# Performance work log

Measured on AMD Instinct MI355X. Metric: run time of the kernel, lower is better.

## Reference

```python
import jax, jax.numpy as jnp
import numpy as np

NUM_CANDIDATES = 9
CENTER_IN_GT = True
MIN_IOU = 0.0
LEVELS = [262144, 32768, 4096, 512]  # anchors per FPN level (static)
NUM_GT = 64


def _to_box(c, s):
    lo = c - s / 2
    hi = c + s / 2
    # layout [x1, y1, x2, y2, z1, z2]
    return jnp.stack([lo[:, 0], lo[:, 1], hi[:, 0], hi[:, 1], lo[:, 2], hi[:, 2]], axis=1)


def setup_inputs() -> dict:
    key = jax.random.key(0)
    k1, k2, k3, k4 = jax.random.split(key, 4)
    n = sum(LEVELS)
    a_ctr = jax.random.uniform(k1, (n, 3), dtype=jnp.float32) * 512.0
    a_sz = jax.random.uniform(k2, (n, 3), dtype=jnp.float32) * 60.0 + 4.0
    g_ctr = jax.random.uniform(k3, (NUM_GT, 3), dtype=jnp.float32) * 512.0
    g_sz = jax.random.uniform(k4, (NUM_GT, 3), dtype=jnp.float32) * 90.0 + 10.0
    return {"gt_boxes": _to_box(g_ctr, g_sz), "anchors": _to_box(a_ctr, a_sz)}


def _centers(b):
    return jnp.stack([(b[:, 0] + b[:, 2]) / 2,
                      (b[:, 1] + b[:, 3]) / 2,
                      (b[:, 4] + b[:, 5]) / 2], axis=1)


def _iou(a, b):
    # a: (N,6), b: (M,6) -> (N,M) 3D IoU
    def vol(x):
        return (x[:, 2] - x[:, 0]) * (x[:, 3] - x[:, 1]) * (x[:, 5] - x[:, 4])
    v1, v2 = vol(a), vol(b)
    wx = jnp.clip(jnp.minimum(a[:, None, 2], b[None, :, 2]) - jnp.maximum(a[:, None, 0], b[None, :, 0]), 0.0)
    wy = jnp.clip(jnp.minimum(a[:, None, 3], b[None, :, 3]) - jnp.maximum(a[:, None, 1], b[None, :, 1]), 0.0)
    wz = jnp.clip(jnp.minimum(a[:, None, 5], b[None, :, 5]) - jnp.maximum(a[:, None, 4], b[None, :, 4]), 0.0)
    inter = wx * wy * wz
    return inter / (v1[:, None] + v2[None, :] - inter + 1e-6)


def reference(gt_boxes, anchors):
    n = anchors.shape[0]
    m = gt_boxes.shape[0]
    a_ctr = _centers(anchors)   # (N,3)
    g_ctr = _centers(gt_boxes)  # (M,3)

    # squared center distance (monotone in L2 distance, so topk ordering identical)
    d2 = ((a_ctr * a_ctr).sum(1)[:, None] + (g_ctr * g_ctr).sum(1)[None, :]
          - 2.0 * a_ctr @ g_ctr.T)  # (N,M)

    # per-level, per-GT top-k nearest anchors -> candidate set (vectorized over all GTs)
    cand_mask = jnp.zeros((n, m), dtype=bool)
    cand_idx_list = []
    gt_ids = jnp.arange(m)[:, None]
    start = 0
    for lvl in LEVELS:
        k = min(NUM_CANDIDATES, lvl)
        d_lvl = d2[start:start + lvl].T            # (M, lvl)
        _, idx = jax.lax.top_k(-d_lvl, k)          # smallest distances
        gidx = idx + start                         # (M, k) global anchor ids
        cand_mask = cand_mask.at[gidx, gt_ids].set(True)
        cand_idx_list.append(gidx)
        start += lvl
    cand_idx = jnp.concatenate(cand_idx_list, axis=1)  # (M, K_total)

    iou = _iou(anchors, gt_boxes)  # (N,M)

    # adaptive threshold per GT: mean + std (torch default: unbiased) over candidates
    cand_iou = jnp.take_along_axis(iou.T, cand_idx, axis=1)  # (M, K_total)
    thr = jnp.maximum(cand_iou.mean(axis=1) + cand_iou.std(axis=1, ddof=1), MIN_IOU)  # (M,)

    pos = cand_mask & (iou >= thr[None, :])
    if CENTER_IN_GT:
        inside = ((a_ctr[:, None, 0] >= gt_boxes[None, :, 0]) & (a_ctr[:, None, 0] <= gt_boxes[None, :, 2]) &
                  (a_ctr[:, None, 1] >= gt_boxes[None, :, 1]) & (a_ctr[:, None, 1] <= gt_boxes[None, :, 3]) &
                  (a_ctr[:, None, 2] >= gt_boxes[None, :, 4]) & (a_ctr[:, None, 2] <= gt_boxes[None, :, 5]))
        pos = pos & inside

    # conflict resolution: the sequential GT loop in the original assigns each anchor
    # to the positive GT with the highest IoU (ties -> earliest GT index) == argmax.
    any_pos = pos.any(axis=1)
    masked_iou = jnp.where(pos, iou, -jnp.inf)
    best = jnp.argmax(masked_iou, axis=1)  # (N,)
    matched_iou = jnp.where(any_pos, jnp.take_along_axis(iou, best[:, None], axis=1)[:, 0], 0.0)
    matched_gt_indices = jnp.where(any_pos, best, -1).astype(jnp.int32)
    labels = (matched_gt_indices >= 0).astype(jnp.int32)
    return matched_gt_indices, matched_iou, labels
```

## Files before the change

### kernel.cpp

```cpp
#include <hip/hip_runtime.h>
#include <cstdint>


#define NCAND 36
#define QCAP 64
#define OVF  0x80000000u
#define LVL1_START 262144
#define LVL2_START 294912
#define LVL3_START 299008
#define SEG0 512
#define SEG1 64

__device__ __constant__ int   c_lvl_start[2] = {0, 262144};
__device__ __constant__ int   c_lvl_end[2]   = {262144, 294912};
__device__ __constant__ float c_T[2] = {961.0f, 3844.0f};

__device__ inline unsigned f2ord(float f) {
    unsigned u = __float_as_uint(f);
    return (u & 0x80000000u) ? ~u : (u | 0x80000000u);
}

__global__ void scanK(const float* __restrict__ anchors, const float* __restrict__ gt_boxes,
                      unsigned long long* __restrict__ l0, unsigned long long* __restrict__ l1,
                      unsigned* __restrict__ c0, unsigned* __restrict__ c1,
                      unsigned long long* __restrict__ packed, int n, int m) {
    int b    = blockIdx.x;
    int tid  = threadIdx.x;
    int base = b << 9;
    int lvl  = (base >= LVL1_START) ? 1 : 0;
    float T  = c_T[lvl];

    int segN = (lvl == 0) ? SEG0 : SEG1;
    int seg  = (lvl == 0) ? b : (b - SEG0);
    unsigned long long* lseg = (lvl == 0) ? l0 : l1;

    __shared__ float4 gt4[64];
    __shared__ unsigned qcnt[64];

    if (tid < 64) {
        qcnt[tid] = 0;
        if (tid < m) {
            int g = tid;
            float gx = (gt_boxes[g*6+0] + gt_boxes[g*6+2]) * 0.5f;
            float gy = (gt_boxes[g*6+1] + gt_boxes[g*6+3]) * 0.5f;
            float gz = (gt_boxes[g*6+4] + gt_boxes[g*6+5]) * 0.5f;
            float sg = gx*gx + gy*gy + gz*gz;
            gt4[g] = make_float4(gx, gy, gz, sg);
        }
    }
    if (b < 9) {
        int s = LVL2_START + (b << 9) + tid;
        if (s < n) packed[s] = 0ULL;
        if (s + 256 < n) packed[s + 256] = 0ULL;
    }
    __syncthreads();

    float ax[2], ay[2], az[2], sa[2];
    int   ai[2];
    #pragma unroll
    for (int k = 0; k < 2; k++) {
        int a = base + tid + k*256;
        ai[k] = a;
        const float2* r = (const float2*)(anchors + (size_t)a*6);
        float2 p0 = r[0], p1 = r[1], p2 = r[2];
        float cx = (p0.x + p1.x) * 0.5f;
        float cy = (p0.y + p1.y) * 0.5f;
        float cz = (p2.x + p2.y) * 0.5f;
        ax[k] = cx; ay[k] = cy; az[k] = cz;
        sa[k] = cx*cx + cy*cy + cz*cz;
        packed[a] = 0ULL;
    }

    for (int g = 0; g < m; g++) {
        float4 gv = gt4[g];
        size_t segoff = ((size_t)g * segN + seg) * QCAP;
        #pragma unroll
        for (int k = 0; k < 2; k++) {
            float dot = ax[k]*gv.x + ay[k]*gv.y + az[k]*gv.z;
            float d2  = sa[k] + gv.w - 2.0f*dot;
            if (d2 <= T) {
                unsigned idx = atomicAdd(&qcnt[g], 1u);
                if (idx < QCAP) {
                    unsigned long long p =
                        ((unsigned long long)f2ord(d2) << 32) | (unsigned)ai[k];
                    lseg[segoff + idx] = p;
                }
            }
        }
    }
    __syncthreads();

    if (tid < 64) {
        unsigned c = qcnt[tid];
        unsigned cw = (c > QCAP) ? OVF : c;
        if (lvl == 0) c0[tid * SEG0 + seg] = cw;
        else          c1[tid * SEG1 + seg] = cw;
    }
}

__global__ void selectC(const unsigned long long* __restrict__ l0,
                        const unsigned long long* __restrict__ l1,
                        const unsigned* __restrict__ c0,
                        const unsigned* __restrict__ c1,
                        const float* __restrict__ anchors,
                        const float* __restrict__ gt_boxes,
                        unsigned long long* __restrict__ packed, int n) {
    int g = blockIdx.x;
    int tid = threadIdx.x;
    int wl  = tid >> 6;
    int lane = tid & 63;
    __shared__ int scand[NCAND];

    float gx1 = gt_boxes[g*6+0], gy1 = gt_boxes[g*6+1];
    float gx2 = gt_boxes[g*6+2], gy2 = gt_boxes[g*6+3];
    float gz1 = gt_boxes[g*6+4], gz2 = gt_boxes[g*6+5];
    float gx = (gx1+gx2)*0.5f, gy = (gy1+gy2)*0.5f, gz = (gz1+gz2)*0.5f;
    float sg = gx*gx + gy*gy + gz*gz;

    unsigned long long e[9];
    #pragma unroll
    for (int k = 0; k < 9; k++) e[k] = ~0ULL;

    if (wl == 3) {
        #pragma unroll
        for (int j = 0; j < 8; j++) {
            int i = LVL3_START + lane + 64*j;
            if (i < n) {
                const float2* r = (const float2*)(anchors + (size_t)i*6);
                float2 p0 = r[0], p1 = r[1], p2 = r[2];
                float cx = (p0.x + p1.x) * 0.5f;
                float cy = (p0.y + p1.y) * 0.5f;
                float cz = (p2.x + p2.y) * 0.5f;
                float sa2 = cx*cx + cy*cy + cz*cz;
                float dot = cx*gx + cy*gy + cz*gz;
                float d2  = sa2 + sg - 2.0f*dot;
                e[j] = ((unsigned long long)f2ord(d2) << 32) | (unsigned)i;
            }
        }
    } else if (wl == 2) {
        for (int i = LVL2_START + lane; i < LVL3_START; i += 64) {
            const float2* r = (const float2*)(anchors + (size_t)i*6);
            float2 p0 = r[0], p1 = r[1], p2 = r[2];
            float cx = (p0.x + p1.x) * 0.5f;
            float cy = (p0.y + p1.y) * 0.5f;
            float cz = (p2.x + p2.y) * 0.5f;
            float sa2 = cx*cx + cy*cy + cz*cz;
            float dot = cx*gx + cy*gy + cz*gz;
            float d2  = sa2 + sg - 2.0f*dot;
            unsigned long long x = ((unsigned long long)f2ord(d2) << 32) | (unsigned)i;
            if (x < e[8]) {
                #pragma unroll
                for (int k = 0; k < 9; k++) {
                    unsigned long long lo = (x < e[k]) ? x : e[k];
                    unsigned long long hi = (x < e[k]) ? e[k] : x;
                    e[k] = lo; x = hi;
                }
            }
        }
    } else {
        int segN = (wl == 0) ? SEG0 : SEG1;
        int J    = (wl == 0) ? 8 : 1;
        const unsigned* cc = (wl == 0) ? c0 : c1;
        const unsigned long long* ll = (wl == 0) ? l0 : l1;

        unsigned cs[8];
        unsigned tot = 0, ovf = 0;
        #pragma unroll
        for (int j = 0; j < 8; j++) {
            cs[j] = 0;
            if (j < J) {
                unsigned c = cc[(size_t)g * segN + lane + 64*j];
                cs[j] = c;
                if (c & OVF) ovf = 1; else tot += c;
            }
        }
        #pragma unroll
        for (int o = 32; o >= 1; o >>= 1) {
            tot += __shfl_xor(tot, o);
            ovf |= __shfl_xor(ovf, o);
        }

        if (!ovf && tot >= 9) {
            #pragma unroll
            for (int j = 0; j < 8; j++) {
                if (j < J) {
                    size_t segoff = ((size_t)g * segN + lane + 64*j) * QCAP;
                    unsigned c = cs[j];
                    for (unsigned s = 0; s < c; s++) {
                        unsigned long long x = ll[segoff + s];
                        if (x < e[8]) {
                            #pragma unroll
                            for (int k = 0; k < 9; k++) {
                                unsigned long long lo = (x < e[k]) ? x : e[k];
                                unsigned long long hi = (x < e[k]) ? e[k] : x;
                                e[k] = lo; x = hi;
                            }
                        }
                    }
                }
            }
        } else {
            int s0 = c_lvl_start[wl], s1 = c_lvl_end[wl];
            for (int i = s0 + lane; i < s1; i += 64) {
                const float2* r = (const float2*)(anchors + (size_t)i*6);
                float2 p0 = r[0], p1 = r[1], p2 = r[2];
                float cx = (p0.x + p1.x) * 0.5f;
                float cy = (p0.y + p1.y) * 0.5f;
                float cz = (p2.x + p2.y) * 0.5f;
                float sa2 = cx*cx + cy*cy + cz*cz;
                float dot = cx*gx + cy*gy + cz*gz;
                float d2  = sa2 + sg - 2.0f*dot;
                unsigned long long x = ((unsigned long long)f2ord(d2) << 32) | (unsigned)i;
                if (x < e[8]) {
                    #pragma unroll
                    for (int k = 0; k < 9; k++) {
                        unsigned long long lo = (x < e[k]) ? x : e[k];
                        unsigned long long hi = (x < e[k]) ? e[k] : x;
                        e[k] = lo; x = hi;
                    }
                }
            }
        }
    }

    #pragma unroll
    for (int r9 = 0; r9 < 9; r9++) {
        unsigned long long mn = e[0];
        #pragma unroll
        for (int j = 1; j < 9; j++) mn = (e[j] < mn) ? e[j] : mn;
        #pragma unroll
        for (int off = 32; off >= 1; off >>= 1) {
            unsigned long long o = __shfl_xor(mn, off);
            mn = (o < mn) ? o : mn;
        }
        if (lane == 0) scand[wl*9 + r9] = (int)(unsigned)mn;
        #pragma unroll
        for (int j = 0; j < 9; j++) e[j] = (e[j] == mn) ? ~0ULL : e[j];
    }
    __syncthreads();

    if (tid < 64) {
        float vg = (gx2 - gx1) * (gy2 - gy1) * (gz2 - gz1);
        bool valid = (tid < NCAND);
        float iou = 0.0f;
        int aidx = 0;
        float acx = 0.0f, acy = 0.0f, acz = 0.0f;
        if (valid) {
            aidx = scand[tid];
            float ax1 = anchors[aidx*6+0], ay1 = anchors[aidx*6+1];
            float ax2 = anchors[aidx*6+2], ay2 = anchors[aidx*6+3];
            float az1 = anchors[aidx*6+4], az2 = anchors[aidx*6+5];
            float va = (ax2 - ax1) * (ay2 - ay1) * (az2 - az1);
            float wx = fmaxf(fminf(ax2, gx2) - fmaxf(ax1, gx1), 0.0f);
            float wy = fmaxf(fminf(ay2, gy2) - fmaxf(ay1, gy1), 0.0f);
            float wz = fmaxf(fminf(az2, gz2) - fmaxf(az1, gz1), 0.0f);
            float inter = wx * wy * wz;
            iou = inter / (va + vg - inter + 1e-6f);
            acx = (ax1 + ax2) * 0.5f;
            acy = (ay1 + ay2) * 0.5f;
            acz = (az1 + az2) * 0.5f;
        }

        float s = iou;
        #pragma unroll
        for (int o = 32; o >= 1; o >>= 1) s += __shfl_xor(s, o);
        float mean = s / 36.0f;
        float dev = valid ? (iou - mean) : 0.0f;
        float s2 = dev * dev;
        #pragma unroll
        for (int o = 32; o >= 1; o >>= 1) s2 += __shfl_xor(s2, o);
        float thr = fmaxf(mean + sqrtf(s2 / 35.0f), 0.0f);

        if (valid && iou >= thr) {
            bool inside = (acx >= gx1) & (acx <= gx2) &
                          (acy >= gy1) & (acy <= gy2) &
                          (acz >= gz1) & (acz <= gz2);
            if (inside) {
                unsigned long long p =
                    ((unsigned long long)__float_as_uint(iou) << 32) | (unsigned)(~(unsigned)g);
                atomicMax(&packed[aidx], p);
            }
        }
    }
}

__global__ void phaseD(const unsigned long long* __restrict__ packed,
                       float* __restrict__ out, int n) {
    int i = blockIdx.x * blockDim.x + threadIdx.x;
    if (i >= n) return;
    unsigned long long p = packed[i];
    float gt_f, iou_f, lab_f;
    if (p == 0ULL) {
        gt_f = -1.0f; iou_f = 0.0f; lab_f = 0.0f;
    } else {
        unsigned low = (unsigned)p;
        int gidx = (int)(~low);
        iou_f = __uint_as_float((unsigned)(p >> 32));
        gt_f = (float)gidx;
        lab_f = 1.0f;
    }
    out[i]       = gt_f;
    out[n + i]   = iou_f;
    out[2*n + i] = lab_f;
}

extern "C" void kernel_launch(void* const* d_in, const int* in_sizes, int n_in,
                              void* d_out, int out_size, void* d_ws, size_t ws_size,
                              hipStream_t stream) {
    const float* gt      = (const float*)d_in[0];
    const float* anchors = (const float*)d_in[1];
    int m = in_sizes[0] / 6;
    int n = in_sizes[1] / 6;

    char* ws = (char*)d_ws;
    unsigned long long* packed = (unsigned long long*)ws;
    size_t off = (size_t)n * 8;
    unsigned long long* l0 = (unsigned long long*)(ws + off);
    off += (size_t)64 * SEG0 * QCAP * 8;
    unsigned long long* l1 = (unsigned long long*)(ws + off);
    off += (size_t)64 * SEG1 * QCAP * 8;
    unsigned* c0 = (unsigned*)(ws + off);
    off += (size_t)64 * SEG0 * 4;
    unsigned* c1 = (unsigned*)(ws + off);
    float* out = (float*)d_out;

    scanK<<<SEG0 + SEG1, 256, 0, stream>>>(anchors, gt, l0, l1, c0, c1, packed, n, m);
    selectC<<<m, 256, 0, stream>>>(l0, l1, c0, c1, anchors, gt, packed, n);
    phaseD<<<(n + 255) / 256, 256, 0, stream>>>(packed, out, n);
}
```

Before: 55.41 us.

## Split level-2 scan across two waves and unroll anchor loads in selectC

```diff
diff --git a/kernel.cpp b/kernel.cpp
--- a/kernel.cpp
+++ b/kernel.cpp
@@ -7,6 +7,7 @@
 #define OVF  0x80000000u
 #define LVL1_START 262144
 #define LVL2_START 294912
+#define LVL2_MID   296960
 #define LVL3_START 299008
 #define SEG0 512
 #define SEG1 64
@@ -15,9 +16,74 @@
 __device__ __constant__ int   c_lvl_end[2]   = {262144, 294912};
 __device__ __constant__ float c_T[2] = {961.0f, 3844.0f};
 
-__device__ inline unsigned f2ord(float f) {
+__device__ __forceinline__ unsigned f2ord(float f) {
     unsigned u = __float_as_uint(f);
     return (u & 0x80000000u) ? ~u : (u | 0x80000000u);
+}
+
+__device__ __forceinline__ void insertChain(unsigned long long e[9], unsigned long long x) {
+    if (x < e[8]) {
+        #pragma unroll
+        for (int k = 0; k < 9; k++) {
+            unsigned long long lo = (x < e[k]) ? x : e[k];
+            unsigned long long hi = (x < e[k]) ? e[k] : x;
+            e[k] = lo; x = hi;
+        }
+    }
+}
+
+__device__ __forceinline__ void waveTop9(unsigned long long e[9], int lane,
+                                         unsigned long long* out9) {
+    #pragma unroll
+    for (int r9 = 0; r9 < 9; r9++) {
+        unsigned long long mn = e[0];
+        #pragma unroll
+        for (int j = 1; j < 9; j++) mn = (e[j] < mn) ? e[j] : mn;
+        #pragma unroll
+        for (int off = 32; off >= 1; off >>= 1) {
+            unsigned long long o = __shfl_xor(mn, off);
+            mn = (o < mn) ? o : mn;
+        }
+        if (lane == 0) out9[r9] = mn;
+        #pragma unroll
+        for (int j = 0; j < 9; j++) e[j] = (e[j] == mn) ? ~0ULL : e[j];
+    }
+}
+
+__device__ __forceinline__ void scanRange(const float* __restrict__ anchors,
+                                          int s0, int s1, int lane,
+                                          float gx, float gy, float gz, float sg,
+                                          unsigned long long e[9]) {
+    int i = s0 + lane;
+    for (; i + 192 < s1; i += 256) {
+        float2 q[4][3];
+        #pragma unroll
+        for (int u = 0; u < 4; u++) {
+            const float2* r = (const float2*)(anchors + (size_t)(i + u*64)*6);
+            q[u][0] = r[0]; q[u][1] = r[1]; q[u][2] = r[2];
+        }
+        #pragma unroll
+        for (int u = 0; u < 4; u++) {
+            float cx = (q[u][0].x + q[u][1].x) * 0.5f;
+            float cy = (q[u][0].y + q[u][1].y) * 0.5f;
+            float cz = (q[u][2].x + q[u][2].y) * 0.5f;
+            float sa2 = cx*cx + cy*cy + cz*cz;
+            float dot = cx*gx + cy*gy + cz*gz;
+            float d2  = sa2 + sg - 2.0f*dot;
+            insertChain(e, ((unsigned long long)f2ord(d2) << 32) | (unsigned)(i + u*64));
+        }
+    }
+    for (; i < s1; i += 64) {
+        const float2* r = (const float2*)(anchors + (size_t)i*6);
+        float2 p0 = r[0], p1 = r[1], p2 = r[2];
+        float cx = (p0.x + p1.x) * 0.5f;
+        float cy = (p0.y + p1.y) * 0.5f;
+        float cz = (p2.x + p2.y) * 0.5f;
+        float sa2 = cx*cx + cy*cy + cz*cz;
+        float dot = cx*gx + cy*gy + cz*gz;
+        float d2  = sa2 + sg - 2.0f*dot;
+        insertChain(e, ((unsigned long long)f2ord(d2) << 32) | (unsigned)i);
+    }
 }
 
 __global__ void scanK(const float* __restrict__ anchors, const float* __restrict__ gt_boxes,
@@ -109,7 +175,8 @@
     int tid = threadIdx.x;
     int wl  = tid >> 6;
     int lane = tid & 63;
-    __shared__ int scand[NCAND];
+    __shared__ unsigned long long cands[NCAND];
+    __shared__ unsigned long long cand2[18];
 
     float gx1 = gt_boxes[g*6+0], gy1 = gt_boxes[g*6+1];
     float gx2 = gt_boxes[g*6+2], gy2 = gt_boxes[g*6+3];
@@ -122,57 +189,36 @@
     for (int k = 0; k < 9; k++) e[k] = ~0ULL;
 
     if (wl == 3) {
-        #pragma unroll
-        for (int j = 0; j < 8; j++) {
-            int i = LVL3_START + lane + 64*j;
-            if (i < n) {
-                const float2* r = (const float2*)(anchors + (size_t)i*6);
-                float2 p0 = r[0], p1 = r[1], p2 = r[2];
-                float cx = (p0.x + p1.x) * 0.5f;
-                float cy = (p0.y + p1.y) * 0.5f;
-                float cz = (p2.x + p2.y) * 0.5f;
-                float sa2 = cx*cx + cy*cy + cz*cz;
-                float dot = cx*gx + cy*gy + cz*gz;
-                float d2  = sa2 + sg - 2.0f*dot;
-                e[j] = ((unsigned long long)f2ord(d2) << 32) | (unsigned)i;
-            }
-        }
+        scanRange(anchors, LVL3_START, n, lane, gx, gy, gz, sg, e);
+        waveTop9(e, lane, &cands[27]);
+        #pragma unroll
+        for (int k = 0; k < 9; k++) e[k] = ~0ULL;
+        scanRange(anchors, LVL2_MID, LVL3_START, lane, gx, gy, gz, sg, e);
+        waveTop9(e, lane, &cand2[9]);
     } else if (wl == 2) {
-        for (int i = LVL2_START + lane; i < LVL3_START; i += 64) {
-            const float2* r = (const float2*)(anchors + (size_t)i*6);
-            float2 p0 = r[0], p1 = r[1], p2 = r[2];
-            float cx = (p0.x + p1.x) * 0.5f;
-            float cy = (p0.y + p1.y) * 0.5f;
-            float cz = (p2.x + p2.y) * 0.5f;
-            float sa2 = cx*cx + cy*cy + cz*cz;
-            float dot = cx*gx + cy*gy + cz*gz;
-            float d2  = sa2 + sg - 2.0f*dot;
-            unsigned long long x = ((unsigned long long)f2ord(d2) << 32) | (unsigned)i;
-            if (x < e[8]) {
-                #pragma unroll
-                for (int k = 0; k < 9; k++) {
-                    unsigned long long lo = (x < e[k]) ? x : e[k];
-                    unsigned long long hi = (x < e[k]) ? e[k] : x;
-                    e[k] = lo; x = hi;
-                }
-            }
-        }
+        scanRange(anchors, LVL2_START, LVL2_MID, lane, gx, gy, gz, sg, e);
+        waveTop9(e, lane, &cand2[0]);
     } else {
         int segN = (wl == 0) ? SEG0 : SEG1;
         int J    = (wl == 0) ? 8 : 1;
         const unsigned* cc = (wl == 0) ? c0 : c1;
         const unsigned long long* ll = (wl == 0) ? l0 : l1;
+        size_t sb = (size_t)g * segN * QCAP;
 
         unsigned cs[8];
+        unsigned long long q0[8];
         unsigned tot = 0, ovf = 0;
         #pragma unroll
         for (int j = 0; j < 8; j++) {
-            cs[j] = 0;
+            cs[j] = 0; q0[j] = ~0ULL;
             if (j < J) {
-                unsigned c = cc[(size_t)g * segN + lane + 64*j];
-                cs[j] = c;
-                if (c & OVF) ovf = 1; else tot += c;
-            }
+                cs[j] = cc[(size_t)g * segN + lane + 64*j];
+                q0[j] = ll[sb + (size_t)(lane + 64*j) * QCAP];
+            }
+        }
+        #pragma unroll
+        for (int j = 0; j < 8; j++) {
+            if (j < J) { if (cs[j] & OVF) ovf = 1; else tot += cs[j]; }
         }
         #pragma unroll
         for (int o = 32; o >= 1; o >>= 1) {
@@ -184,58 +230,33 @@
             #pragma unroll
             for (int j = 0; j < 8; j++) {
                 if (j < J) {
-                    size_t segoff = ((size_t)g * segN + lane + 64*j) * QCAP;
                     unsigned c = cs[j];
-                    for (unsigned s = 0; s < c; s++) {
-                        unsigned long long x = ll[segoff + s];
-                        if (x < e[8]) {
-                            #pragma unroll
-                            for (int k = 0; k < 9; k++) {
-                                unsigned long long lo = (x < e[k]) ? x : e[k];
-                                unsigned long long hi = (x < e[k]) ? e[k] : x;
-                                e[k] = lo; x = hi;
-                            }
-                        }
-                    }
+                    if (c >= 1) insertChain(e, q0[j]);
+                    size_t segoff = sb + (size_t)(lane + 64*j) * QCAP;
+                    for (unsigned s = 1; s < c; s++)
+                        insertChain(e, ll[segoff + s]);
                 }
             }
         } else {
-            int s0 = c_lvl_start[wl], s1 = c_lvl_end[wl];
-            for (int i = s0 + lane; i < s1; i += 64) {
-                const float2* r = (const float2*)(anchors + (size_t)i*6);
-                float2 p0 = r[0], p1 = r[1], p2 = r[2];
-                float cx = (p0.x + p1.x) * 0.5f;
-                float cy = (p0.y + p1.y) * 0.5f;
-                float cz = (p2.x + p2.y) * 0.5f;
-                float sa2 = cx*cx + cy*cy + cz*cz;
-                float dot = cx*gx + cy*gy + cz*gz;
-                float d2  = sa2 + sg - 2.0f*dot;
-                unsigned long long x = ((unsigned long long)f2ord(d2) << 32) | (unsigned)i;
-                if (x < e[8]) {
-                    #pragma unroll
-                    for (int k = 0; k < 9; k++) {
-                        unsigned long long lo = (x < e[k]) ? x : e[k];
-                        unsigned long long hi = (x < e[k]) ? e[k] : x;
-                        e[k] = lo; x = hi;
-                    }
-                }
-            }
-        }
-    }
-
-    #pragma unroll
-    for (int r9 = 0; r9 < 9; r9++) {
-        unsigned long long mn = e[0];
-        #pragma unroll
-        for (int j = 1; j < 9; j++) mn = (e[j] < mn) ? e[j] : mn;
-        #pragma unroll
-        for (int off = 32; off >= 1; off >>= 1) {
-            unsigned long long o = __shfl_xor(mn, off);
-            mn = (o < mn) ? o : mn;
-        }
-        if (lane == 0) scand[wl*9 + r9] = (int)(unsigned)mn;
-        #pragma unroll
-        for (int j = 0; j < 9; j++) e[j] = (e[j] == mn) ? ~0ULL : e[j];
+            scanRange(anchors, c_lvl_start[wl], c_lvl_end[wl], lane, gx, gy, gz, sg, e);
+        }
+        waveTop9(e, lane, &cands[wl*9]);
+    }
+    __syncthreads();
+
+    if (wl == 2) {
+        unsigned long long v = (lane < 18) ? cand2[lane] : ~0ULL;
+        #pragma unroll
+        for (int r9 = 0; r9 < 9; r9++) {
+            unsigned long long mn = v;
+            #pragma unroll
+            for (int off = 32; off >= 1; off >>= 1) {
+                unsigned long long o = __shfl_xor(mn, off);
+                mn = (o < mn) ? o : mn;
+            }
+            if (lane == 0) cands[18 + r9] = mn;
+            v = (v == mn) ? ~0ULL : v;
+        }
     }
     __syncthreads();
 
@@ -246,7 +267,7 @@
         int aidx = 0;
         float acx = 0.0f, acy = 0.0f, acz = 0.0f;
         if (valid) {
-            aidx = scand[tid];
+            aidx = (int)(unsigned)cands[tid];
             float ax1 = anchors[aidx*6+0], ay1 = anchors[aidx*6+1];
             float ax2 = anchors[aidx*6+2], ay2 = anchors[aidx*6+3];
             float az1 = anchors[aidx*6+4], az2 = anchors[aidx*6+5];
```

Result: faster. 46.62 us (-15.9%).
